# Kernel optimization log

Hardware: AMD Instinct MI355X
Metric: run time of the kernel (lower is better)

## Reference

```python
import jax, jax.numpy as jnp
import numpy as np

N = 20000          # nodes
E = 320000         # edges
H = 128            # hidden_channels
A = 512            # aerial feature dim
SPOT = 20000
DIST_UNIT = 50
NEMB = SPOT // DIST_UNIT
RATIO = 0.25       # neighbor_ratio


def setup_inputs() -> dict:
    key = jax.random.key(0)
    ks = jax.random.split(key, 12)
    x = jax.random.normal(ks[0], (N, H), jnp.float32)
    edge_index = jax.random.randint(ks[1], (2, E), 0, N)
    distances = jax.random.randint(ks[2], (E,), 0, SPOT)
    aerial_emb = jax.random.normal(ks[3], (N, A), jnp.float32)
    s = lambda k, shape, fan: jax.random.normal(k, shape, jnp.float32) / np.sqrt(fan).astype(np.float32)
    W_lin = s(ks[4], (H, H), H)
    b_lin = jnp.zeros((H,), jnp.float32)
    W_q = s(ks[5], (H + A + H, H), H + A + H)
    b_q = jnp.zeros((H,), jnp.float32)
    W_v = s(ks[6], (H, H), H)
    b_v = jnp.zeros((H,), jnp.float32)
    dist_table = jax.random.normal(ks[7], (NEMB, H), jnp.float32)  # init.normal_ like torch
    W_l = s(ks[8], (H, H), H)   # SAGE lin_l (neighbor aggr), with bias
    b_l = jnp.zeros((H,), jnp.float32)
    W_r = s(ks[9], (H, H), H)   # SAGE lin_r (root), no bias in PyG default
    return dict(x=x, edge_index=edge_index, distances=distances, aerial_emb=aerial_emb,
                W_lin=W_lin, b_lin=b_lin, W_q=W_q, b_q=b_q, W_v=W_v, b_v=b_v,
                dist_table=dist_table, W_l=W_l, b_l=b_l, W_r=W_r)


def reference(x, edge_index, distances, aerial_emb, W_lin, b_lin, W_q, b_q, W_v, b_v, dist_table, W_l, b_l, W_r):
    n = x.shape[0]
    e = edge_index.shape[1]
    k = int(e * RATIO)  # static: number of sampled edges

    x = x @ W_lin + b_lin                                  # [N, H]
    src, tgt = edge_index[0], edge_index[1]
    source_x = x[src]                                      # [E, H]
    target_x = x[tgt]                                      # [E, H]
    source_aerial = aerial_emb[src]                        # [E, A]
    dist_x = dist_table[distances // DIST_UNIT]            # [E, H]

    query = jnp.concatenate([source_x, source_aerial, dist_x], axis=1) @ W_q + b_q  # [E, H]
    value = target_x @ W_v + b_v                           # [E, H]
    logits = -jnp.linalg.norm(query - value, axis=1)       # [E]
    logprob = jax.nn.log_softmax(logits, axis=0)

    # torch.multinomial(prob, k) without replacement == Gumbel top-k on log-probs
    u = jax.random.uniform(jax.random.key(42), (e,), jnp.float32)
    gumbel = -jnp.log(-jnp.log(u + 1e-20) + 1e-20)
    _, sel = jax.lax.top_k(logprob + gumbel, k)            # [k] selected edge ids
    src_s = src[sel]
    tgt_s = tgt[sel]

    # SAGEConv (mean aggregation): out = lin_l(mean_j x_j) + lin_r(x)
    msg = jax.ops.segment_sum(x[src_s], tgt_s, num_segments=n)              # [N, H]
    deg = jax.ops.segment_sum(jnp.ones((k,), x.dtype), tgt_s, num_segments=n)
    aggr = msg / jnp.maximum(deg, 1.0)[:, None]
    out = aggr @ W_l + b_l + x @ W_r                       # [N, H]
    return out
```

## Files before the change

### kernel.cpp

```cpp
#include <hip/hip_runtime.h>
#include <stdint.h>

#define N_NODES 20000
#define E_EDGES 320000
#define H_DIM 128
#define A_DIM 512
#define NEMB_N 400
#define K_SEL 80000u
#define NB1 16384
#define NB2 16384
#define CAND_MAX 8192
#define LO_F (-128.0f)
#define SCALE1 (16384.0f / 160.0f)

struct SelState {
    int b1; unsigned cum1; unsigned r1;
    int b2; unsigned cum2; unsigned r2;
    unsigned long long T;
};

__device__ __forceinline__ uint32_t rotl32(uint32_t x, int r) {
    return (x << r) | (x >> (32 - r));
}

__device__ __forceinline__ void threefry2x32(uint32_t k0, uint32_t k1,
                                             uint32_t& x0, uint32_t& x1) {
    uint32_t ks0 = k0, ks1 = k1, ks2 = k0 ^ k1 ^ 0x1BD11BDAu;
    x0 += ks0; x1 += ks1;
    x0 += x1; x1 = rotl32(x1, 13); x1 ^= x0;
    x0 += x1; x1 = rotl32(x1, 15); x1 ^= x0;
    x0 += x1; x1 = rotl32(x1, 26); x1 ^= x0;
    x0 += x1; x1 = rotl32(x1, 6);  x1 ^= x0;
    x0 += ks1; x1 += ks2 + 1u;
    x0 += x1; x1 = rotl32(x1, 17); x1 ^= x0;
    x0 += x1; x1 = rotl32(x1, 29); x1 ^= x0;
    x0 += x1; x1 = rotl32(x1, 16); x1 ^= x0;
    x0 += x1; x1 = rotl32(x1, 24); x1 ^= x0;
    x0 += ks2; x1 += ks0 + 2u;
    x0 += x1; x1 = rotl32(x1, 13); x1 ^= x0;
    x0 += x1; x1 = rotl32(x1, 15); x1 ^= x0;
    x0 += x1; x1 = rotl32(x1, 26); x1 ^= x0;
    x0 += x1; x1 = rotl32(x1, 6);  x1 ^= x0;
    x0 += ks0; x1 += ks1 + 3u;
    x0 += x1; x1 = rotl32(x1, 17); x1 ^= x0;
    x0 += x1; x1 = rotl32(x1, 29); x1 ^= x0;
    x0 += x1; x1 = rotl32(x1, 16); x1 ^= x0;
    x0 += x1; x1 = rotl32(x1, 24); x1 ^= x0;
    x0 += ks1; x1 += ks2 + 4u;
    x0 += x1; x1 = rotl32(x1, 13); x1 ^= x0;
    x0 += x1; x1 = rotl32(x1, 15); x1 ^= x0;
    x0 += x1; x1 = rotl32(x1, 26); x1 ^= x0;
    x0 += x1; x1 = rotl32(x1, 6);  x1 ^= x0;
    x0 += ks2; x1 += ks0 + 5u;
}

__global__ __launch_bounds__(256) void k_rand(float* __restrict__ u) {
    int e = blockIdx.x * 256 + threadIdx.x;
    if (e >= E_EDGES) return;
    uint32_t x0 = 0u, x1 = (uint32_t)e;
    threefry2x32(0u, 42u, x0, x1);
    uint32_t bits = x0 ^ x1;
    uint32_t fb = (bits >> 9) | 0x3f800000u;
    u[e] = __uint_as_float(fb) - 1.0f;
}

__global__ __launch_bounds__(128) void k_node(
    const float* __restrict__ x, const float* __restrict__ aerial,
    const float* __restrict__ Wlin, const float* __restrict__ blin,
    const float* __restrict__ Wq, const float* __restrict__ bq,
    const float* __restrict__ Wv, const float* __restrict__ bv,
    float* __restrict__ xl32, float* __restrict__ q32, float* __restrict__ v32) {
    __shared__ float xinT[H_DIM][8];
    __shared__ float xsT[H_DIM][8];
    __shared__ float aerT[A_DIM][8];
    const int j = threadIdx.x;
    const int n0 = blockIdx.x * 8;
#pragma unroll
    for (int m = 0; m < 8; ++m) xinT[j][m] = x[(size_t)(n0 + m) * H_DIM + j];
#pragma unroll
    for (int m = 0; m < 8; ++m)
#pragma unroll
        for (int c = 0; c < 4; ++c)
            aerT[c * H_DIM + j][m] = aerial[(size_t)(n0 + m) * A_DIM + c * H_DIM + j];
    __syncthreads();
    float acc[8];
    {
        float bj = blin[j];
#pragma unroll
        for (int m = 0; m < 8; ++m) acc[m] = bj;
        for (int k = 0; k < H_DIM; ++k) {
            float w = Wlin[k * H_DIM + j];
            const float4* xp = (const float4*)&xinT[k][0];
            float4 a0 = xp[0], a1 = xp[1];
            acc[0] = fmaf(a0.x, w, acc[0]); acc[1] = fmaf(a0.y, w, acc[1]);
            acc[2] = fmaf(a0.z, w, acc[2]); acc[3] = fmaf(a0.w, w, acc[3]);
            acc[4] = fmaf(a1.x, w, acc[4]); acc[5] = fmaf(a1.y, w, acc[5]);
            acc[6] = fmaf(a1.z, w, acc[6]); acc[7] = fmaf(a1.w, w, acc[7]);
        }
    }
#pragma unroll
    for (int m = 0; m < 8; ++m) {
        xsT[j][m] = acc[m];
        xl32[(size_t)(n0 + m) * H_DIM + j] = acc[m];
    }
    __syncthreads();
    {
        float bj = bv[j];
        float av[8];
#pragma unroll
        for (int m = 0; m < 8; ++m) av[m] = bj;
        for (int k = 0; k < H_DIM; ++k) {
            float w = Wv[k * H_DIM + j];
            const float4* xp = (const float4*)&xsT[k][0];
            float4 a0 = xp[0], a1 = xp[1];
            av[0] = fmaf(a0.x, w, av[0]); av[1] = fmaf(a0.y, w, av[1]);
            av[2] = fmaf(a0.z, w, av[2]); av[3] = fmaf(a0.w, w, av[3]);
            av[4] = fmaf(a1.x, w, av[4]); av[5] = fmaf(a1.y, w, av[5]);
            av[6] = fmaf(a1.z, w, av[6]); av[7] = fmaf(a1.w, w, av[7]);
        }
#pragma unroll
        for (int m = 0; m < 8; ++m) v32[(size_t)(n0 + m) * H_DIM + j] = av[m];
    }
    {
        float bj = bq[j];
        float aq[8];
#pragma unroll
        for (int m = 0; m < 8; ++m) aq[m] = bj;
        for (int k = 0; k < H_DIM; ++k) {
            float w = Wq[k * H_DIM + j];
            const float4* xp = (const float4*)&xsT[k][0];
            float4 a0 = xp[0], a1 = xp[1];
            aq[0] = fmaf(a0.x, w, aq[0]); aq[1] = fmaf(a0.y, w, aq[1]);
            aq[2] = fmaf(a0.z, w, aq[2]); aq[3] = fmaf(a0.w, w, aq[3]);
            aq[4] = fmaf(a1.x, w, aq[4]); aq[5] = fmaf(a1.y, w, aq[5]);
            aq[6] = fmaf(a1.z, w, aq[6]); aq[7] = fmaf(a1.w, w, aq[7]);
        }
        for (int k = 0; k < A_DIM; ++k) {
            float w = Wq[(size_t)(H_DIM + k) * H_DIM + j];
            const float4* xp = (const float4*)&aerT[k][0];
            float4 a0 = xp[0], a1 = xp[1];
            aq[0] = fmaf(a0.x, w, aq[0]); aq[1] = fmaf(a0.y, w, aq[1]);
            aq[2] = fmaf(a0.z, w, aq[2]); aq[3] = fmaf(a0.w, w, aq[3]);
            aq[4] = fmaf(a1.x, w, aq[4]); aq[5] = fmaf(a1.y, w, aq[5]);
            aq[6] = fmaf(a1.z, w, aq[6]); aq[7] = fmaf(a1.w, w, aq[7]);
        }
#pragma unroll
        for (int m = 0; m < 8; ++m) q32[(size_t)(n0 + m) * H_DIM + j] = aq[m];
    }
}

__global__ __launch_bounds__(128) void k_dist(
    const float* __restrict__ dtab, const float* __restrict__ Wq,
    float* __restrict__ dq32) {
    __shared__ float dsT[H_DIM][8];
    const int j = threadIdx.x;
    const int n0 = blockIdx.x * 8;
#pragma unroll
    for (int m = 0; m < 8; ++m) dsT[j][m] = dtab[(size_t)(n0 + m) * H_DIM + j];
    __syncthreads();
    float acc[8];
#pragma unroll
    for (int m = 0; m < 8; ++m) acc[m] = 0.0f;
    for (int k = 0; k < H_DIM; ++k) {
        float w = Wq[(size_t)(H_DIM + A_DIM + k) * H_DIM + j];
        const float4* xp = (const float4*)&dsT[k][0];
        float4 a0 = xp[0], a1 = xp[1];
        acc[0] = fmaf(a0.x, w, acc[0]); acc[1] = fmaf(a0.y, w, acc[1]);
        acc[2] = fmaf(a0.z, w, acc[2]); acc[3] = fmaf(a0.w, w, acc[3]);
        acc[4] = fmaf(a1.x, w, acc[4]); acc[5] = fmaf(a1.y, w, acc[5]);
        acc[6] = fmaf(a1.z, w, acc[6]); acc[7] = fmaf(a1.w, w, acc[7]);
    }
#pragma unroll
    for (int m = 0; m < 8; ++m) dq32[(size_t)(n0 + m) * H_DIM + j] = acc[m];
}

__device__ __forceinline__ int bin1_of(float s) {
    float t = (s - LO_F) * SCALE1;
    int b = (int)t;
    return min(max(b, 0), NB1 - 1);
}
__device__ __forceinline__ int bin2_of(float s, int b1) {
    float t = (s - LO_F) * SCALE1;
    float frac = t - (float)b1;
    int b = (int)(frac * (float)NB2);
    return min(max(b, 0), NB2 - 1);
}

__global__ __launch_bounds__(256) void k_score(
    const int* __restrict__ ei, const int* __restrict__ dist,
    const float* __restrict__ q32, const float* __restrict__ v32,
    const float* __restrict__ dq32, const float* __restrict__ u,
    unsigned long long* __restrict__ keys, float* __restrict__ s32o,
    unsigned* __restrict__ hist1) {
    const int g = threadIdx.x >> 5, lane = threadIdx.x & 31;
    const int e0 = blockIdx.x * 32 + g * 4;

    const int s0 = ei[e0 + 0], s1 = ei[e0 + 1], s2 = ei[e0 + 2], s3 = ei[e0 + 3];
    const int t0 = ei[E_EDGES + e0 + 0], t1 = ei[E_EDGES + e0 + 1];
    const int t2 = ei[E_EDGES + e0 + 2], t3 = ei[E_EDGES + e0 + 3];
    const int d0 = dist[e0 + 0] / 50, d1 = dist[e0 + 1] / 50;
    const int d2 = dist[e0 + 2] / 50, d3 = dist[e0 + 3] / 50;

    float4 q0 = ((const float4*)(q32 + (size_t)s0 * H_DIM))[lane];
    float4 q1 = ((const float4*)(q32 + (size_t)s1 * H_DIM))[lane];
    float4 q2 = ((const float4*)(q32 + (size_t)s2 * H_DIM))[lane];
    float4 q3 = ((const float4*)(q32 + (size_t)s3 * H_DIM))[lane];
    float4 v0 = ((const float4*)(v32 + (size_t)t0 * H_DIM))[lane];
    float4 v1 = ((const float4*)(v32 + (size_t)t1 * H_DIM))[lane];
    float4 v2 = ((const float4*)(v32 + (size_t)t2 * H_DIM))[lane];
    float4 v3 = ((const float4*)(v32 + (size_t)t3 * H_DIM))[lane];
    float4 w0 = ((const float4*)(dq32 + (size_t)d0 * H_DIM))[lane];
    float4 w1 = ((const float4*)(dq32 + (size_t)d1 * H_DIM))[lane];
    float4 w2 = ((const float4*)(dq32 + (size_t)d2 * H_DIM))[lane];
    float4 w3 = ((const float4*)(dq32 + (size_t)d3 * H_DIM))[lane];

    float ax, ay, az, aw;
    ax = q0.x + w0.x - v0.x; ay = q0.y + w0.y - v0.y;
    az = q0.z + w0.z - v0.z; aw = q0.w + w0.w - v0.w;
    float ss0 = fmaf(ax, ax, fmaf(ay, ay, fmaf(az, az, aw * aw)));
    ax = q1.x + w1.x - v1.x; ay = q1.y + w1.y - v1.y;
    az = q1.z + w1.z - v1.z; aw = q1.w + w1.w - v1.w;
    float ss1 = fmaf(ax, ax, fmaf(ay, ay, fmaf(az, az, aw * aw)));
    ax = q2.x + w2.x - v2.x; ay = q2.y + w2.y - v2.y;
    az = q2.z + w2.z - v2.z; aw = q2.w + w2.w - v2.w;
    float ss2 = fmaf(ax, ax, fmaf(ay, ay, fmaf(az, az, aw * aw)));
    ax = q3.x + w3.x - v3.x; ay = q3.y + w3.y - v3.y;
    az = q3.z + w3.z - v3.z; aw = q3.w + w3.w - v3.w;
    float ss3 = fmaf(ax, ax, fmaf(ay, ay, fmaf(az, az, aw * aw)));

#pragma unroll
    for (int o = 16; o > 0; o >>= 1) {
        ss0 += __shfl_xor(ss0, o, 64);
        ss1 += __shfl_xor(ss1, o, 64);
        ss2 += __shfl_xor(ss2, o, 64);
        ss3 += __shfl_xor(ss3, o, 64);
    }
    if (lane < 4) {
        float ssv = (lane == 0) ? ss0 : (lane == 1) ? ss1 : (lane == 2) ? ss2 : ss3;
        const int e = e0 + lane;
        float nrm = sqrtf(ssv);
        float uu = u[e];
        float a = -logf(uu + 1e-20f);
        float gm = -logf(a + 1e-20f);
        float score = gm - nrm;
        int ib = __float_as_int(score);
        unsigned m32 = (ib < 0) ? ~(unsigned)ib : ((unsigned)ib | 0x80000000u);
        keys[e] = ((unsigned long long)m32 << 32) | (unsigned)(0xFFFFFFFFu - (unsigned)e);
        s32o[e] = score;
        atomicAdd(&hist1[bin1_of(score)], 1u);
    }
}

__global__ __launch_bounds__(256) void k_hist2(const float* __restrict__ s32,
                                               const SelState* __restrict__ st,
                                               unsigned* __restrict__ hist2) {
    int e = blockIdx.x * 256 + threadIdx.x;
    if (e >= E_EDGES) return;
    float s = s32[e];
    int b1 = bin1_of(s);
    if (b1 != st->b1) return;
    atomicAdd(&hist2[bin2_of(s, b1)], 1u);
}

__global__ __launch_bounds__(256) void k_scan(const unsigned* __restrict__ hist,
                                              SelState* st, int phase) {
    __shared__ unsigned csum[256];
    __shared__ unsigned bins[64];
    __shared__ int selc;
    __shared__ unsigned cumbase;
    const int t = threadIdx.x;
    const unsigned target = (phase == 1) ? K_SEL : st->r1;
    unsigned s = 0;
    for (int i = 0; i < 64; ++i) s += hist[t * 64 + i];
    csum[t] = s;
    __syncthreads();
    if (t == 0) {
        unsigned cum = 0; int c = 255;
        for (; c >= 0; --c) {
            if (cum + csum[c] >= target) break;
            cum += csum[c];
        }
        selc = c; cumbase = cum;
    }
    __syncthreads();
    if (t < 64) bins[t] = hist[selc * 64 + t];
    __syncthreads();
    if (t == 0) {
        unsigned cum = cumbase; int b = -1;
        for (int i = 63; i >= 0; --i) {
            if (cum + bins[i] >= target) { b = selc * 64 + i; break; }
            cum += bins[i];
        }
        unsigned r = target - cum;
        if (phase == 1) { st->b1 = b; st->cum1 = cum; st->r1 = r; }
        else           { st->b2 = b; st->cum2 = cum; st->r2 = r; }
    }
}

__global__ __launch_bounds__(256) void k_collect(
    const float* __restrict__ s32, const unsigned long long* __restrict__ keys,
    const SelState* __restrict__ st, unsigned long long* __restrict__ cand,
    unsigned* __restrict__ cnt) {
    int e = blockIdx.x * 256 + threadIdx.x;
    if (e >= E_EDGES) return;
    float s = s32[e];
    int b1 = bin1_of(s);
    if (b1 != st->b1) return;
    if (bin2_of(s, b1) != st->b2) return;
    unsigned p = atomicAdd(cnt, 1u);
    if (p < CAND_MAX) cand[p] = keys[e];
}

__global__ __launch_bounds__(256) void k_thresh(
    const unsigned long long* __restrict__ cand, const unsigned* __restrict__ cnt,
    SelState* st) {
    int c = (int)min(*cnt, (unsigned)CAND_MAX);
    unsigned r2 = st->r2;
    for (int i = threadIdx.x; i < c; i += blockDim.x) {
        unsigned long long ki = cand[i];
        unsigned g = 0;
        for (int j = 0; j < c; ++j) g += (cand[j] > ki);
        if (g == r2 - 1) st->T = ki;
    }
}

__global__ __launch_bounds__(256) void k_scatter(
    const int* __restrict__ ei, const unsigned long long* __restrict__ keys,
    const SelState* __restrict__ st, const float* __restrict__ xl32,
    float* __restrict__ msg, float* __restrict__ deg) {
    const int wid = threadIdx.x >> 6, lane = threadIdx.x & 63;
    const int e = blockIdx.x * 4 + wid;
    if (keys[e] >= st->T) {
        int sidx = ei[e], tidx = ei[E_EDGES + e];
        const float* xp = xl32 + (size_t)sidx * H_DIM;
        float* mp = msg + (size_t)tidx * H_DIM;
        const int h = lane * 2;
        atomicAdd(&mp[h], xp[h]);
        atomicAdd(&mp[h + 1], xp[h + 1]);
        if (lane == 0) atomicAdd(&deg[tidx], 1.0f);
    }
}

__global__ __launch_bounds__(128) void k_out(
    const float* __restrict__ msg, const float* __restrict__ deg,
    const float* __restrict__ xl32, const float* __restrict__ Wl,
    const float* __restrict__ bl, const float* __restrict__ Wr,
    float* __restrict__ out) {
    __shared__ float axT[H_DIM][8];
    __shared__ float xxT[H_DIM][8];
    const int j = threadIdx.x;
    const int n0 = blockIdx.x * 8;
#pragma unroll
    for (int m = 0; m < 8; ++m) {
        float d = fmaxf(deg[n0 + m], 1.0f);
        axT[j][m] = msg[(size_t)(n0 + m) * H_DIM + j] / d;
        xxT[j][m] = xl32[(size_t)(n0 + m) * H_DIM + j];
    }
    __syncthreads();
    float acc[8];
    float bj = bl[j];
#pragma unroll
    for (int m = 0; m < 8; ++m) acc[m] = bj;
    for (int k = 0; k < H_DIM; ++k) {
        float wl = Wl[k * H_DIM + j];
        float wr = Wr[k * H_DIM + j];
        const float4* ap = (const float4*)&axT[k][0];
        const float4* xp = (const float4*)&xxT[k][0];
        float4 a0 = ap[0], a1 = ap[1];
        float4 x0 = xp[0], x1 = xp[1];
        acc[0] = fmaf(a0.x, wl, fmaf(x0.x, wr, acc[0]));
        acc[1] = fmaf(a0.y, wl, fmaf(x0.y, wr, acc[1]));
        acc[2] = fmaf(a0.z, wl, fmaf(x0.z, wr, acc[2]));
        acc[3] = fmaf(a0.w, wl, fmaf(x0.w, wr, acc[3]));
        acc[4] = fmaf(a1.x, wl, fmaf(x1.x, wr, acc[4]));
        acc[5] = fmaf(a1.y, wl, fmaf(x1.y, wr, acc[5]));
        acc[6] = fmaf(a1.z, wl, fmaf(x1.z, wr, acc[6]));
        acc[7] = fmaf(a1.w, wl, fmaf(x1.w, wr, acc[7]));
    }
#pragma unroll
    for (int m = 0; m < 8; ++m) out[(size_t)(n0 + m) * H_DIM + j] = acc[m];
}

extern "C" void kernel_launch(void* const* d_in, const int* in_sizes, int n_in,
                              void* d_out, int out_size, void* d_ws, size_t ws_size,
                              hipStream_t stream) {
    const float* x      = (const float*)d_in[0];
    const int*   ei     = (const int*)d_in[1];
    const int*   dist   = (const int*)d_in[2];
    const float* aerial = (const float*)d_in[3];
    const float* Wlin   = (const float*)d_in[4];
    const float* blin   = (const float*)d_in[5];
    const float* Wq     = (const float*)d_in[6];
    const float* bq     = (const float*)d_in[7];
    const float* Wv     = (const float*)d_in[8];
    const float* bv     = (const float*)d_in[9];
    const float* dtab   = (const float*)d_in[10];
    const float* Wl     = (const float*)d_in[11];
    const float* bl     = (const float*)d_in[12];
    const float* Wr     = (const float*)d_in[13];
    float* out = (float*)d_out;

    char* ws = (char*)d_ws;
    size_t off = 0;
    auto alloc = [&](size_t bytes) -> void* {
        void* p = ws + off;
        off += (bytes + 255) & ~(size_t)255;
        return p;
    };
    float* q32  = (float*)alloc((size_t)N_NODES * H_DIM * 4);
    float* v32  = (float*)alloc((size_t)N_NODES * H_DIM * 4);
    float* dq32 = (float*)alloc((size_t)NEMB_N * H_DIM * 4);
    unsigned long long* keys = (unsigned long long*)alloc((size_t)E_EDGES * 8);
    float* xl32 = (float*)alloc((size_t)N_NODES * H_DIM * 4);
    float* urnd = (float*)alloc((size_t)E_EDGES * 4);
    float* s32  = (float*)alloc((size_t)E_EDGES * 4);
    char* zbase = ws + off;
    float* msg  = (float*)alloc((size_t)N_NODES * H_DIM * 4);
    float* deg  = (float*)alloc((size_t)N_NODES * 4);
    unsigned* hist1 = (unsigned*)alloc((size_t)NB1 * 4);
    unsigned* hist2 = (unsigned*)alloc((size_t)NB2 * 4);
    unsigned long long* cand = (unsigned long long*)alloc((size_t)CAND_MAX * 8);
    unsigned* counters = (unsigned*)alloc(256);
    SelState* st = (SelState*)alloc(256);
    size_t zlen = (size_t)((ws + off) - zbase);

    hipMemsetAsync(zbase, 0, zlen, stream);

    k_node<<<N_NODES / 8, 128, 0, stream>>>(x, aerial, Wlin, blin, Wq, bq, Wv, bv,
                                            xl32, q32, v32);
    k_dist<<<NEMB_N / 8, 128, 0, stream>>>(dtab, Wq, dq32);
    k_rand<<<(E_EDGES + 255) / 256, 256, 0, stream>>>(urnd);
    k_score<<<E_EDGES / 32, 256, 0, stream>>>(ei, dist, q32, v32, dq32, urnd, keys, s32, hist1);
    k_scan<<<1, 256, 0, stream>>>(hist1, st, 1);
    k_hist2<<<(E_EDGES + 255) / 256, 256, 0, stream>>>(s32, st, hist2);
    k_scan<<<1, 256, 0, stream>>>(hist2, st, 2);
    k_collect<<<(E_EDGES + 255) / 256, 256, 0, stream>>>(s32, keys, st, cand, &counters[0]);
    k_thresh<<<1, 256, 0, stream>>>(cand, &counters[0], st);
    k_scatter<<<E_EDGES / 4, 256, 0, stream>>>(ei, keys, st, xl32, msg, deg);
    k_out<<<N_NODES / 8, 128, 0, stream>>>(msg, deg, xl32, Wl, bl, Wr, out);
}
```

Before: 535.0 us.

## Replace atomic scatter with CSR-by-target gather aggregation and widen node blocks

The float-atomic scatter of selected edges into msg/deg is replaced by a counting sort by target: count selected edges per target, prefix-sum them in a single block, place source ids, then do a per-node gather-and-mean with one wavefront per node. This removes about 10M float atomics and the large memset of msg, at the cost of three extra small kernels, including a serial single-block prefix. Separately, k_node and k_out now process 16 nodes per 256-thread block instead of 8 per 128, which doubles the reuse of each weight load. Summation order inside a node now depends on atomic placement order, so results are not bitwise deterministic.

```diff
diff --git a/kernel.cpp b/kernel.cpp
--- a/kernel.cpp
+++ b/kernel.cpp
@@ -64,24 +64,28 @@
     u[e] = __uint_as_float(fb) - 1.0f;
 }
 
-__global__ __launch_bounds__(128) void k_node(
+__global__ __launch_bounds__(256) void k_node(
     const float* __restrict__ x, const float* __restrict__ aerial,
     const float* __restrict__ Wlin, const float* __restrict__ blin,
     const float* __restrict__ Wq, const float* __restrict__ bq,
     const float* __restrict__ Wv, const float* __restrict__ bv,
     float* __restrict__ xl32, float* __restrict__ q32, float* __restrict__ v32) {
-    __shared__ float xinT[H_DIM][8];
-    __shared__ float xsT[H_DIM][8];
-    __shared__ float aerT[A_DIM][8];
-    const int j = threadIdx.x;
-    const int n0 = blockIdx.x * 8;
-#pragma unroll
-    for (int m = 0; m < 8; ++m) xinT[j][m] = x[(size_t)(n0 + m) * H_DIM + j];
+    __shared__ float xinT[H_DIM][16];
+    __shared__ float xsT[H_DIM][16];
+    __shared__ float aerT[A_DIM][16];
+    const int j = threadIdx.x & 127;
+    const int h = threadIdx.x >> 7;
+    const int mb = h * 8;
+    const int n0 = blockIdx.x * 16;
 #pragma unroll
     for (int m = 0; m < 8; ++m)
+        xinT[j][mb + m] = x[(size_t)(n0 + mb + m) * H_DIM + j];
+#pragma unroll
+    for (int m = 0; m < 8; ++m)
 #pragma unroll
         for (int c = 0; c < 4; ++c)
-            aerT[c * H_DIM + j][m] = aerial[(size_t)(n0 + m) * A_DIM + c * H_DIM + j];
+            aerT[c * H_DIM + j][mb + m] =
+                aerial[(size_t)(n0 + mb + m) * A_DIM + c * H_DIM + j];
     __syncthreads();
     float acc[8];
     {
@@ -90,7 +94,7 @@
         for (int m = 0; m < 8; ++m) acc[m] = bj;
         for (int k = 0; k < H_DIM; ++k) {
             float w = Wlin[k * H_DIM + j];
-            const float4* xp = (const float4*)&xinT[k][0];
+            const float4* xp = (const float4*)&xinT[k][mb];
             float4 a0 = xp[0], a1 = xp[1];
             acc[0] = fmaf(a0.x, w, acc[0]); acc[1] = fmaf(a0.y, w, acc[1]);
             acc[2] = fmaf(a0.z, w, acc[2]); acc[3] = fmaf(a0.w, w, acc[3]);
@@ -100,8 +104,8 @@
     }
 #pragma unroll
     for (int m = 0; m < 8; ++m) {
-        xsT[j][m] = acc[m];
-        xl32[(size_t)(n0 + m) * H_DIM + j] = acc[m];
+        xsT[j][mb + m] = acc[m];
+        xl32[(size_t)(n0 + mb + m) * H_DIM + j] = acc[m];
     }
     __syncthreads();
     {
@@ -111,7 +115,7 @@
         for (int m = 0; m < 8; ++m) av[m] = bj;
         for (int k = 0; k < H_DIM; ++k) {
             float w = Wv[k * H_DIM + j];
-            const float4* xp = (const float4*)&xsT[k][0];
+            const float4* xp = (const float4*)&xsT[k][mb];
             float4 a0 = xp[0], a1 = xp[1];
             av[0] = fmaf(a0.x, w, av[0]); av[1] = fmaf(a0.y, w, av[1]);
             av[2] = fmaf(a0.z, w, av[2]); av[3] = fmaf(a0.w, w, av[3]);
@@ -119,7 +123,8 @@
             av[6] = fmaf(a1.z, w, av[6]); av[7] = fmaf(a1.w, w, av[7]);
         }
 #pragma unroll
-        for (int m = 0; m < 8; ++m) v32[(size_t)(n0 + m) * H_DIM + j] = av[m];
+        for (int m = 0; m < 8; ++m)
+            v32[(size_t)(n0 + mb + m) * H_DIM + j] = av[m];
     }
     {
         float bj = bq[j];
@@ -128,7 +133,7 @@
         for (int m = 0; m < 8; ++m) aq[m] = bj;
         for (int k = 0; k < H_DIM; ++k) {
             float w = Wq[k * H_DIM + j];
-            const float4* xp = (const float4*)&xsT[k][0];
+            const float4* xp = (const float4*)&xsT[k][mb];
             float4 a0 = xp[0], a1 = xp[1];
             aq[0] = fmaf(a0.x, w, aq[0]); aq[1] = fmaf(a0.y, w, aq[1]);
             aq[2] = fmaf(a0.z, w, aq[2]); aq[3] = fmaf(a0.w, w, aq[3]);
@@ -137,7 +142,7 @@
         }
         for (int k = 0; k < A_DIM; ++k) {
             float w = Wq[(size_t)(H_DIM + k) * H_DIM + j];
-            const float4* xp = (const float4*)&aerT[k][0];
+            const float4* xp = (const float4*)&aerT[k][mb];
             float4 a0 = xp[0], a1 = xp[1];
             aq[0] = fmaf(a0.x, w, aq[0]); aq[1] = fmaf(a0.y, w, aq[1]);
             aq[2] = fmaf(a0.z, w, aq[2]); aq[3] = fmaf(a0.w, w, aq[3]);
@@ -145,7 +150,8 @@
             aq[6] = fmaf(a1.z, w, aq[6]); aq[7] = fmaf(a1.w, w, aq[7]);
         }
 #pragma unroll
-        for (int m = 0; m < 8; ++m) q32[(size_t)(n0 + m) * H_DIM + j] = aq[m];
+        for (int m = 0; m < 8; ++m)
+            q32[(size_t)(n0 + mb + m) * H_DIM + j] = aq[m];
     }
 }
 
@@ -324,37 +330,84 @@
     }
 }
 
-__global__ __launch_bounds__(256) void k_scatter(
+__global__ __launch_bounds__(256) void k_selcnt(
     const int* __restrict__ ei, const unsigned long long* __restrict__ keys,
-    const SelState* __restrict__ st, const float* __restrict__ xl32,
-    float* __restrict__ msg, float* __restrict__ deg) {
+    const SelState* __restrict__ st, unsigned* __restrict__ cnt_tgt) {
+    int e = blockIdx.x * 256 + threadIdx.x;
+    if (e >= E_EDGES) return;
+    if (keys[e] >= st->T) atomicAdd(&cnt_tgt[ei[E_EDGES + e]], 1u);
+}
+
+__global__ __launch_bounds__(256) void k_prefix(
+    const unsigned* __restrict__ cnt, unsigned* __restrict__ off,
+    unsigned* __restrict__ off2) {
+    __shared__ unsigned ssum[256];
+    const int t = threadIdx.x;
+    const int PER = (N_NODES + 255) / 256;
+    unsigned s = 0;
+    for (int i = 0; i < PER; ++i) {
+        int idx = t * PER + i;
+        if (idx < N_NODES) s += cnt[idx];
+    }
+    ssum[t] = s;
+    __syncthreads();
+    if (t == 0) {
+        unsigned acc = 0;
+        for (int i = 0; i < 256; ++i) { unsigned v = ssum[i]; ssum[i] = acc; acc += v; }
+    }
+    __syncthreads();
+    unsigned run = ssum[t];
+    for (int i = 0; i < PER; ++i) {
+        int idx = t * PER + i;
+        if (idx < N_NODES) { off[idx] = run; off2[idx] = run; run += cnt[idx]; }
+    }
+}
+
+__global__ __launch_bounds__(256) void k_selplace(
+    const int* __restrict__ ei, const unsigned long long* __restrict__ keys,
+    const SelState* __restrict__ st, unsigned* __restrict__ off_work,
+    int* __restrict__ selsrc) {
+    int e = blockIdx.x * 256 + threadIdx.x;
+    if (e >= E_EDGES) return;
+    if (keys[e] >= st->T) {
+        unsigned p = atomicAdd(&off_work[ei[E_EDGES + e]], 1u);
+        if (p < K_SEL) selsrc[p] = ei[e];
+    }
+}
+
+__global__ __launch_bounds__(256) void k_aggr(
+    const unsigned* __restrict__ cnt_tgt, const unsigned* __restrict__ off_tgt,
+    const int* __restrict__ selsrc, const float* __restrict__ xl32,
+    float* __restrict__ aggr) {
     const int wid = threadIdx.x >> 6, lane = threadIdx.x & 63;
-    const int e = blockIdx.x * 4 + wid;
-    if (keys[e] >= st->T) {
-        int sidx = ei[e], tidx = ei[E_EDGES + e];
-        const float* xp = xl32 + (size_t)sidx * H_DIM;
-        float* mp = msg + (size_t)tidx * H_DIM;
-        const int h = lane * 2;
-        atomicAdd(&mp[h], xp[h]);
-        atomicAdd(&mp[h + 1], xp[h + 1]);
-        if (lane == 0) atomicAdd(&deg[tidx], 1.0f);
-    }
-}
-
-__global__ __launch_bounds__(128) void k_out(
-    const float* __restrict__ msg, const float* __restrict__ deg,
-    const float* __restrict__ xl32, const float* __restrict__ Wl,
-    const float* __restrict__ bl, const float* __restrict__ Wr,
-    float* __restrict__ out) {
-    __shared__ float axT[H_DIM][8];
-    __shared__ float xxT[H_DIM][8];
-    const int j = threadIdx.x;
-    const int n0 = blockIdx.x * 8;
+    const int n = blockIdx.x * 4 + wid;
+    const int cnt = (int)cnt_tgt[n];
+    const unsigned start = off_tgt[n];
+    float ax = 0.0f, ay = 0.0f;
+    for (int i = 0; i < cnt; ++i) {
+        int s = selsrc[start + i];
+        const float2 v = ((const float2*)(xl32 + (size_t)s * H_DIM))[lane];
+        ax += v.x; ay += v.y;
+    }
+    float dm = fmaxf((float)cnt, 1.0f);
+    float2 o; o.x = ax / dm; o.y = ay / dm;
+    ((float2*)(aggr + (size_t)n * H_DIM))[lane] = o;
+}
+
+__global__ __launch_bounds__(256) void k_out(
+    const float* __restrict__ aggr, const float* __restrict__ xl32,
+    const float* __restrict__ Wl, const float* __restrict__ bl,
+    const float* __restrict__ Wr, float* __restrict__ out) {
+    __shared__ float axT[H_DIM][16];
+    __shared__ float xxT[H_DIM][16];
+    const int j = threadIdx.x & 127;
+    const int h = threadIdx.x >> 7;
+    const int mb = h * 8;
+    const int n0 = blockIdx.x * 16;
 #pragma unroll
     for (int m = 0; m < 8; ++m) {
-        float d = fmaxf(deg[n0 + m], 1.0f);
-        axT[j][m] = msg[(size_t)(n0 + m) * H_DIM + j] / d;
-        xxT[j][m] = xl32[(size_t)(n0 + m) * H_DIM + j];
+        axT[j][mb + m] = aggr[(size_t)(n0 + mb + m) * H_DIM + j];
+        xxT[j][mb + m] = xl32[(size_t)(n0 + mb + m) * H_DIM + j];
     }
     __syncthreads();
     float acc[8];
@@ -364,8 +417,8 @@
     for (int k = 0; k < H_DIM; ++k) {
         float wl = Wl[k * H_DIM + j];
         float wr = Wr[k * H_DIM + j];
-        const float4* ap = (const float4*)&axT[k][0];
-        const float4* xp = (const float4*)&xxT[k][0];
+        const float4* ap = (const float4*)&axT[k][mb];
+        const float4* xp = (const float4*)&xxT[k][mb];
         float4 a0 = ap[0], a1 = ap[1];
         float4 x0 = xp[0], x1 = xp[1];
         acc[0] = fmaf(a0.x, wl, fmaf(x0.x, wr, acc[0]));
@@ -378,7 +431,8 @@
         acc[7] = fmaf(a1.w, wl, fmaf(x1.w, wr, acc[7]));
     }
 #pragma unroll
-    for (int m = 0; m < 8; ++m) out[(size_t)(n0 + m) * H_DIM + j] = acc[m];
+    for (int m = 0; m < 8; ++m)
+        out[(size_t)(n0 + mb + m) * H_DIM + j] = acc[m];
 }
 
 extern "C" void kernel_launch(void* const* d_in, const int* in_sizes, int n_in,
@@ -414,28 +468,35 @@
     float* xl32 = (float*)alloc((size_t)N_NODES * H_DIM * 4);
     float* urnd = (float*)alloc((size_t)E_EDGES * 4);
     float* s32  = (float*)alloc((size_t)E_EDGES * 4);
+    float* aggr = (float*)alloc((size_t)N_NODES * H_DIM * 4);
+    int* selsrc = (int*)alloc((size_t)K_SEL * 4);
+    unsigned* off_tgt  = (unsigned*)alloc((size_t)N_NODES * 4);
+    unsigned* off_work = (unsigned*)alloc((size_t)N_NODES * 4);
+    unsigned long long* cand = (unsigned long long*)alloc((size_t)CAND_MAX * 8);
     char* zbase = ws + off;
-    float* msg  = (float*)alloc((size_t)N_NODES * H_DIM * 4);
-    float* deg  = (float*)alloc((size_t)N_NODES * 4);
+    unsigned* cnt_tgt = (unsigned*)alloc((size_t)N_NODES * 4);
     unsigned* hist1 = (unsigned*)alloc((size_t)NB1 * 4);
     unsigned* hist2 = (unsigned*)alloc((size_t)NB2 * 4);
-    unsigned long long* cand = (unsigned long long*)alloc((size_t)CAND_MAX * 8);
     unsigned* counters = (unsigned*)alloc(256);
     SelState* st = (SelState*)alloc(256);
     size_t zlen = (size_t)((ws + off) - zbase);
 
     hipMemsetAsync(zbase, 0, zlen, stream);
 
-    k_node<<<N_NODES / 8, 128, 0, stream>>>(x, aerial, Wlin, blin, Wq, bq, Wv, bv,
-                                            xl32, q32, v32);
+    k_node<<<N_NODES / 16, 256, 0, stream>>>(x, aerial, Wlin, blin, Wq, bq, Wv, bv,
+                                             xl32, q32, v32);
     k_dist<<<NEMB_N / 8, 128, 0, stream>>>(dtab, Wq, dq32);
     k_rand<<<(E_EDGES + 255) / 256, 256, 0, stream>>>(urnd);
-    k_score<<<E_EDGES / 32, 256, 0, stream>>>(ei, dist, q32, v32, dq32, urnd, keys, s32, hist1);
+    k_score<<<E_EDGES / 32, 256, 0, stream>>>(ei, dist, q32, v32, dq32, urnd,
+                                              keys, s32, hist1);
     k_scan<<<1, 256, 0, stream>>>(hist1, st, 1);
     k_hist2<<<(E_EDGES + 255) / 256, 256, 0, stream>>>(s32, st, hist2);
     k_scan<<<1, 256, 0, stream>>>(hist2, st, 2);
     k_collect<<<(E_EDGES + 255) / 256, 256, 0, stream>>>(s32, keys, st, cand, &counters[0]);
     k_thresh<<<1, 256, 0, stream>>>(cand, &counters[0], st);
-    k_scatter<<<E_EDGES / 4, 256, 0, stream>>>(ei, keys, st, xl32, msg, deg);
-    k_out<<<N_NODES / 8, 128, 0, stream>>>(msg, deg, xl32, Wl, bl, Wr, out);
-}
+    k_selcnt<<<(E_EDGES + 255) / 256, 256, 0, stream>>>(ei, keys, st, cnt_tgt);
+    k_prefix<<<1, 256, 0, stream>>>(cnt_tgt, off_tgt, off_work);
+    k_selplace<<<(E_EDGES + 255) / 256, 256, 0, stream>>>(ei, keys, st, off_work, selsrc);
+    k_aggr<<<N_NODES / 4, 256, 0, stream>>>(cnt_tgt, off_tgt, selsrc, xl32, aggr);
+    k_out<<<N_NODES / 16, 256, 0, stream>>>(aggr, xl32, Wl, bl, Wr, out);
+}
```

After: 553.4 us. 1.03x slower.
